# Kernel tuning notes

Hardware: AMD Instinct MI355X
Metric: run time of the kernel (lower is better)

The kernel has to match this reference:

```python
import jax, jax.numpy as jnp
import numpy as np

NUM_POINTS = 2048
FEAT_DIMS = 512
BATCH = 32


def setup_inputs() -> dict:
    key = jax.random.key(0)
    ks = jax.random.split(key, 7)
    glf = jax.random.normal(ks[0], (BATCH, FEAT_DIMS, 1), dtype=jnp.float32)
    # Per-position linear weights (one Conv1d(k=1) per position, fused):
    # W[p, out, in], b[p, out]. Scale like PyTorch Conv1d default init.
    W1 = jax.random.normal(ks[1], (NUM_POINTS, 32, FEAT_DIMS), dtype=jnp.float32) * (1.0 / np.sqrt(FEAT_DIMS))
    b1 = jax.random.normal(ks[2], (NUM_POINTS, 32), dtype=jnp.float32) * 0.01
    W2 = jax.random.normal(ks[3], (NUM_POINTS, 8, 32), dtype=jnp.float32) * (1.0 / np.sqrt(32))
    b2 = jax.random.normal(ks[4], (NUM_POINTS, 8), dtype=jnp.float32) * 0.01
    W3 = jax.random.normal(ks[5], (NUM_POINTS, 3, 8), dtype=jnp.float32) * (1.0 / np.sqrt(8))
    b3 = jax.random.normal(ks[6], (NUM_POINTS, 3), dtype=jnp.float32) * 0.01
    return {"glf": glf, "W1": W1, "b1": b1, "W2": W2, "b2": b2, "W3": W3, "b3": b3}


def _fc_layer(x, W, b):
    # x: [B, Cin, P], W: [P, Cout, Cin], b: [P, Cout] -> [B, Cout, P]
    return jnp.einsum('bip,poi->bop', x, W) + b.T[None, :, :]


def reference(glf, W1, b1, W2, b2, W3, b3):
    # glf: [B, feat_dims, 1] -> repeat along positions
    x = jnp.broadcast_to(glf, (glf.shape[0], glf.shape[1], NUM_POINTS))
    x = _fc_layer(x, W1, b1)  # [B, 32, P]
    x = _fc_layer(x, W2, b2)  # [B, 8, P]
    x = _fc_layer(x, W3, b3)  # [B, 3, P]  (seg_class == 0)
    return x
```

## Files before the change

### kernel.cpp

```cpp
#include <hip/hip_runtime.h>

#define NUM_POINTS 2048
#define FEAT 512
#define BATCH 32
#define POS_PER_BLOCK 4

using v8s = __attribute__((ext_vector_type(8))) short;
using v4f = __attribute__((ext_vector_type(4))) float;

static __device__ __forceinline__ short f2bf(float x) {
  unsigned u = __float_as_uint(x);
  u += 0x7FFFu + ((u >> 16) & 1u);
  return (short)(u >> 16);
}

__global__ void build_bfrag(const float* __restrict__ glf, short* __restrict__ frag) {
  int i = blockIdx.x * 256 + threadIdx.x;
  int j = i & 7;
  int l = (i >> 3) & 63;
  int nt = (i >> 9) & 1;
  int ks = i >> 10;
  int b = nt * 16 + (l & 15);
  int k = ks * 32 + ((l >> 4) << 3) + j;
  frag[i] = f2bf(glf[b * FEAT + k]);
}

__global__ void __launch_bounds__(256) fcdec_main(
    const float* __restrict__ W1, const float* __restrict__ b1,
    const float* __restrict__ W2, const float* __restrict__ b2,
    const float* __restrict__ W3, const float* __restrict__ b3,
    const short* __restrict__ bfrag, float* __restrict__ out) {
  __shared__ float h1s[POS_PER_BLOCK][32][33];
  const int t = threadIdx.x;
  const int w = t >> 6;
  const int l = t & 63;
  const int p = blockIdx.x * POS_PER_BLOCK + w;
  const int lrow = l & 15;
  const int lk = (l >> 4) << 3;

  v4f acc[2][2] = {};
  const float* A0 = W1 + (size_t)p * 32u * FEAT;

  #pragma unroll 4
  for (int ks = 0; ks < 16; ++ks) {
    v8s a[2];
    #pragma unroll
    for (int mt = 0; mt < 2; ++mt) {
      const float* ap = A0 + (size_t)(mt * 16 + lrow) * FEAT + ks * 32 + lk;
      float4 f0 = *(const float4*)(ap);
      float4 f1 = *(const float4*)(ap + 4);
      v8s av;
      av[0] = f2bf(f0.x); av[1] = f2bf(f0.y); av[2] = f2bf(f0.z); av[3] = f2bf(f0.w);
      av[4] = f2bf(f1.x); av[5] = f2bf(f1.y); av[6] = f2bf(f1.z); av[7] = f2bf(f1.w);
      a[mt] = av;
    }
    #pragma unroll
    for (int nt = 0; nt < 2; ++nt) {
      v8s bv = *(const v8s*)(bfrag + (((ks * 2 + nt) * 64 + l) << 3));
      acc[0][nt] = __builtin_amdgcn_mfma_f32_16x16x32_bf16(a[0], bv, acc[0][nt], 0, 0, 0);
      acc[1][nt] = __builtin_amdgcn_mfma_f32_16x16x32_bf16(a[1], bv, acc[1][nt], 0, 0, 0);
    }
  }

  #pragma unroll
  for (int mt = 0; mt < 2; ++mt)
    #pragma unroll
    for (int nt = 0; nt < 2; ++nt)
      #pragma unroll
      for (int r = 0; r < 4; ++r) {
        int o = mt * 16 + ((l >> 4) << 2) + r;
        int b = nt * 16 + (l & 15);
        h1s[w][o][b] = acc[mt][nt][r] + b1[p * 32 + o];
      }
  __syncthreads();

  if (t < POS_PER_BLOCK * 32) {
    int lp = t >> 5;
    int b = t & 31;
    int pg = blockIdx.x * POS_PER_BLOCK + lp;
    float h2[8];
    #pragma unroll
    for (int o8 = 0; o8 < 8; ++o8) {
      float s = b2[pg * 8 + o8];
      const float* w2 = W2 + (size_t)(pg * 8 + o8) * 32;
      #pragma unroll
      for (int i = 0; i < 32; ++i) s += w2[i] * h1s[lp][i][b];
      h2[o8] = s;
    }
    #pragma unroll
    for (int c = 0; c < 3; ++c) {
      float s = b3[pg * 3 + c];
      const float* w3 = W3 + (size_t)(pg * 3 + c) * 8;
      #pragma unroll
      for (int j = 0; j < 8; ++j) s += w3[j] * h2[j];
      out[(size_t)(b * 3 + c) * NUM_POINTS + pg] = s;
    }
  }
}

extern "C" void kernel_launch(void* const* d_in, const int* in_sizes, int n_in,
                              void* d_out, int out_size, void* d_ws, size_t ws_size,
                              hipStream_t stream) {
  const float* glf = (const float*)d_in[0];
  const float* W1  = (const float*)d_in[1];
  const float* b1  = (const float*)d_in[2];
  const float* W2  = (const float*)d_in[3];
  const float* b2  = (const float*)d_in[4];
  const float* W3  = (const float*)d_in[5];
  const float* b3  = (const float*)d_in[6];
  float* out = (float*)d_out;
  short* frag = (short*)d_ws;

  hipLaunchKernelGGL(build_bfrag, dim3(64), dim3(256), 0, stream, glf, frag);
  hipLaunchKernelGGL(fcdec_main, dim3(NUM_POINTS / POS_PER_BLOCK), dim3(256), 0, stream,
                     W1, b1, W2, b2, W3, b3, frag, out);
}
```

Baseline: 34.40 us.

## Split K across waves per position and fuse glf conversion into main kernel

Each block now handles one position, and its four waves each take a quarter of the 512-long K dimension. Partial accumulators are reduced through shared memory before the small layer-2/3 MLP runs. The separate build_bfrag launch is dropped: each wave loads and converts glf to bf16 inline. This is meant to raise parallelism and memory-level concurrency on streaming W1 and to remove a kernel launch. The cost is an extra LDS reduction with two barriers, redundant glf conversion in every block, and only 32 threads active in the tail.

```diff
diff --git a/kernel.cpp b/kernel.cpp
--- a/kernel.cpp
+++ b/kernel.cpp
@@ -3,7 +3,6 @@
 #define NUM_POINTS 2048
 #define FEAT 512
 #define BATCH 32
-#define POS_PER_BLOCK 4
 
 using v8s = __attribute__((ext_vector_type(8))) short;
 using v4f = __attribute__((ext_vector_type(4))) float;
@@ -14,52 +13,46 @@
   return (short)(u >> 16);
 }
 
-__global__ void build_bfrag(const float* __restrict__ glf, short* __restrict__ frag) {
-  int i = blockIdx.x * 256 + threadIdx.x;
-  int j = i & 7;
-  int l = (i >> 3) & 63;
-  int nt = (i >> 9) & 1;
-  int ks = i >> 10;
-  int b = nt * 16 + (l & 15);
-  int k = ks * 32 + ((l >> 4) << 3) + j;
-  frag[i] = f2bf(glf[b * FEAT + k]);
+static __device__ __forceinline__ v8s cvt8(const float* p) {
+  float4 f0 = *(const float4*)(p);
+  float4 f1 = *(const float4*)(p + 4);
+  v8s r;
+  r[0] = f2bf(f0.x); r[1] = f2bf(f0.y); r[2] = f2bf(f0.z); r[3] = f2bf(f0.w);
+  r[4] = f2bf(f1.x); r[5] = f2bf(f1.y); r[6] = f2bf(f1.z); r[7] = f2bf(f1.w);
+  return r;
 }
 
-__global__ void __launch_bounds__(256) fcdec_main(
+__global__ void __launch_bounds__(256, 4) fcdec_main(
+    const float* __restrict__ glf,
     const float* __restrict__ W1, const float* __restrict__ b1,
     const float* __restrict__ W2, const float* __restrict__ b2,
     const float* __restrict__ W3, const float* __restrict__ b3,
-    const short* __restrict__ bfrag, float* __restrict__ out) {
-  __shared__ float h1s[POS_PER_BLOCK][32][33];
+    float* __restrict__ out) {
+  __shared__ float red[4][16][64];
+  __shared__ float h1s[32][33];
+
   const int t = threadIdx.x;
   const int w = t >> 6;
   const int l = t & 63;
-  const int p = blockIdx.x * POS_PER_BLOCK + w;
+  const int p = blockIdx.x;
   const int lrow = l & 15;
   const int lk = (l >> 4) << 3;
 
   v4f acc[2][2] = {};
   const float* A0 = W1 + (size_t)p * 32u * FEAT;
 
-  #pragma unroll 4
-  for (int ks = 0; ks < 16; ++ks) {
-    v8s a[2];
-    #pragma unroll
-    for (int mt = 0; mt < 2; ++mt) {
-      const float* ap = A0 + (size_t)(mt * 16 + lrow) * FEAT + ks * 32 + lk;
-      float4 f0 = *(const float4*)(ap);
-      float4 f1 = *(const float4*)(ap + 4);
-      v8s av;
-      av[0] = f2bf(f0.x); av[1] = f2bf(f0.y); av[2] = f2bf(f0.z); av[3] = f2bf(f0.w);
-      av[4] = f2bf(f1.x); av[5] = f2bf(f1.y); av[6] = f2bf(f1.z); av[7] = f2bf(f1.w);
-      a[mt] = av;
-    }
-    #pragma unroll
-    for (int nt = 0; nt < 2; ++nt) {
-      v8s bv = *(const v8s*)(bfrag + (((ks * 2 + nt) * 64 + l) << 3));
-      acc[0][nt] = __builtin_amdgcn_mfma_f32_16x16x32_bf16(a[0], bv, acc[0][nt], 0, 0, 0);
-      acc[1][nt] = __builtin_amdgcn_mfma_f32_16x16x32_bf16(a[1], bv, acc[1][nt], 0, 0, 0);
-    }
+  #pragma unroll
+  for (int kk = 0; kk < 4; ++kk) {
+    const int ks = w * 4 + kk;
+    const int k0 = ks * 32 + lk;
+    v8s a0 = cvt8(A0 + (size_t)(0 * 16 + lrow) * FEAT + k0);
+    v8s a1 = cvt8(A0 + (size_t)(1 * 16 + lrow) * FEAT + k0);
+    v8s bv0 = cvt8(glf + (size_t)(0 * 16 + lrow) * FEAT + k0);
+    v8s bv1 = cvt8(glf + (size_t)(1 * 16 + lrow) * FEAT + k0);
+    acc[0][0] = __builtin_amdgcn_mfma_f32_16x16x32_bf16(a0, bv0, acc[0][0], 0, 0, 0);
+    acc[0][1] = __builtin_amdgcn_mfma_f32_16x16x32_bf16(a0, bv1, acc[0][1], 0, 0, 0);
+    acc[1][0] = __builtin_amdgcn_mfma_f32_16x16x32_bf16(a1, bv0, acc[1][0], 0, 0, 0);
+    acc[1][1] = __builtin_amdgcn_mfma_f32_16x16x32_bf16(a1, bv1, acc[1][1], 0, 0, 0);
   }
 
   #pragma unroll
@@ -67,33 +60,42 @@
     #pragma unroll
     for (int nt = 0; nt < 2; ++nt)
       #pragma unroll
-      for (int r = 0; r < 4; ++r) {
-        int o = mt * 16 + ((l >> 4) << 2) + r;
-        int b = nt * 16 + (l & 15);
-        h1s[w][o][b] = acc[mt][nt][r] + b1[p * 32 + o];
-      }
+      for (int r = 0; r < 4; ++r)
+        red[w][mt * 8 + nt * 4 + r][l] = acc[mt][nt][r];
   __syncthreads();
 
-  if (t < POS_PER_BLOCK * 32) {
-    int lp = t >> 5;
-    int b = t & 31;
-    int pg = blockIdx.x * POS_PER_BLOCK + lp;
+  {
+    const int c = t >> 6;
+    #pragma unroll
+    for (int j = 0; j < 4; ++j) {
+      const int idx = c * 4 + j;
+      float s = red[0][idx][l] + red[1][idx][l] + red[2][idx][l] + red[3][idx][l];
+      const int mt = idx >> 3, nt = (idx >> 2) & 1, r = idx & 3;
+      const int o = mt * 16 + ((l >> 4) << 2) + r;
+      const int bc = nt * 16 + (l & 15);
+      h1s[o][bc] = s + b1[p * 32 + o];
+    }
+  }
+  __syncthreads();
+
+  if (t < BATCH) {
+    const int b = t;
     float h2[8];
     #pragma unroll
     for (int o8 = 0; o8 < 8; ++o8) {
-      float s = b2[pg * 8 + o8];
-      const float* w2 = W2 + (size_t)(pg * 8 + o8) * 32;
+      float s = b2[p * 8 + o8];
+      const float* w2 = W2 + (size_t)(p * 8 + o8) * 32;
       #pragma unroll
-      for (int i = 0; i < 32; ++i) s += w2[i] * h1s[lp][i][b];
+      for (int i = 0; i < 32; ++i) s += w2[i] * h1s[i][b];
       h2[o8] = s;
     }
     #pragma unroll
     for (int c = 0; c < 3; ++c) {
-      float s = b3[pg * 3 + c];
-      const float* w3 = W3 + (size_t)(pg * 3 + c) * 8;
+      float s = b3[p * 3 + c];
+      const float* w3 = W3 + (size_t)(p * 3 + c) * 8;
       #pragma unroll
       for (int j = 0; j < 8; ++j) s += w3[j] * h2[j];
-      out[(size_t)(b * 3 + c) * NUM_POINTS + pg] = s;
+      out[(size_t)(b * 3 + c) * NUM_POINTS + p] = s;
     }
   }
 }
@@ -109,9 +111,7 @@
   const float* W3  = (const float*)d_in[5];
   const float* b3  = (const float*)d_in[6];
   float* out = (float*)d_out;
-  short* frag = (short*)d_ws;
 
-  hipLaunchKernelGGL(build_bfrag, dim3(64), dim3(256), 0, stream, glf, frag);
-  hipLaunchKernelGGL(fcdec_main, dim3(NUM_POINTS / POS_PER_BLOCK), dim3(256), 0, stream,
-                     W1, b1, W2, b2, W3, b3, frag, out);
+  hipLaunchKernelGGL(fcdec_main, dim3(NUM_POINTS), dim3(256), 0, stream,
+                     glf, W1, b1, W2, b2, W3, b3, out);
 }
```

New measurement: 41.60 us. 20.9% more time.
